# Kernel optimization log

Hardware: AMD Instinct MI355X
Metric: run time of the kernel (lower is better)

## Reference

```python
import jax, jax.numpy as jnp
import numpy as np

H = 8          # num_heads
EPS = 1e-5     # nn.LayerNorm default eps


def _attn(x, kv, wq, bq, wk, bk, wv, bv, wo, bo):
    # x: [B, Nq, D] queries; kv: [B, Nk, D] keys/values. softmax over keys (dim=-1).
    B, Nq, D = x.shape
    Nk = kv.shape[1]
    d = D // H
    q = (x @ wq + bq).reshape(B, Nq, H, d).transpose(0, 2, 1, 3)   # [B,h,Nq,d]
    k = (kv @ wk + bk).reshape(B, Nk, H, d).transpose(0, 2, 1, 3)  # [B,h,Nk,d]
    v = (kv @ wv + bv).reshape(B, Nk, H, d).transpose(0, 2, 1, 3)  # [B,h,Nk,d]
    scores = jnp.einsum('bhqd,bhkd->bhqk', q, k) * (d ** -0.5)
    a = jax.nn.softmax(scores, axis=-1)                            # softmax_dim='keys'
    ctx = jnp.einsum('bhqk,bhkd->bhqd', a, v)
    ctx = ctx.transpose(0, 2, 1, 3).reshape(B, Nq, D)
    return ctx @ wo + bo


def _ln(x, g, b):
    mu = jnp.mean(x, axis=-1, keepdims=True)
    var = jnp.var(x, axis=-1, keepdims=True)  # biased, matches torch LayerNorm
    return (x - mu) * jax.lax.rsqrt(var + EPS) * g + b


def setup_inputs() -> dict:
    key = jax.random.key(0)
    B, Nq, Nk, D = 2, 2048, 4096, 512
    Hid = 4 * D
    ks = jax.random.split(key, 32)
    s = 0.02
    r = lambda i, shp: jax.random.normal(ks[i], shp, dtype=jnp.float32) * s
    inp = {
        'x': jax.random.normal(ks[0], (B, Nq, D), dtype=jnp.float32),
        'cross': jax.random.normal(ks[1], (B, Nk, D), dtype=jnp.float32),
        # cross-attention projections (stored as [in, out])
        'ca_wq': r(2, (D, D)), 'ca_bq': jnp.zeros((D,), jnp.float32),
        'ca_wk': r(3, (D, D)), 'ca_bk': jnp.zeros((D,), jnp.float32),
        'ca_wv': r(4, (D, D)), 'ca_bv': jnp.zeros((D,), jnp.float32),
        'ca_wo': r(5, (D, D)), 'ca_bo': jnp.zeros((D,), jnp.float32),
        # self-attention projections
        'sa_wq': r(6, (D, D)), 'sa_bq': jnp.zeros((D,), jnp.float32),
        'sa_wk': r(7, (D, D)), 'sa_bk': jnp.zeros((D,), jnp.float32),
        'sa_wv': r(8, (D, D)), 'sa_bv': jnp.zeros((D,), jnp.float32),
        'sa_wo': r(9, (D, D)), 'sa_bo': jnp.zeros((D,), jnp.float32),
        # layer norms
        'ln1_g': jnp.ones((D,), jnp.float32), 'ln1_b': jnp.zeros((D,), jnp.float32),
        'ln2_g': jnp.ones((D,), jnp.float32), 'ln2_b': jnp.zeros((D,), jnp.float32),
        # MLP
        'mlp_w1': r(10, (D, Hid)), 'mlp_b1': jnp.zeros((Hid,), jnp.float32),
        'mlp_w2': r(11, (Hid, D)), 'mlp_b2': jnp.zeros((D,), jnp.float32),
    }
    return inp


def reference(x, cross,
              ca_wq, ca_bq, ca_wk, ca_bk, ca_wv, ca_bv, ca_wo, ca_bo,
              sa_wq, sa_bq, sa_wk, sa_bk, sa_wv, sa_bv, sa_wo, sa_bo,
              ln1_g, ln1_b, ln2_g, ln2_b,
              mlp_w1, mlp_b1, mlp_w2, mlp_b2):
    # a) cross-attention
    xc = _attn(x, cross, ca_wq, ca_bq, ca_wk, ca_bk, ca_wv, ca_bv, ca_wo, ca_bo)
    # b,c) LN then self-attention (Q=K=V=ln1(xc))
    xn = _ln(xc, ln1_g, ln1_b)
    xs = _attn(xn, xn, sa_wq, sa_bq, sa_wk, sa_bk, sa_wv, sa_bv, sa_wo, sa_bo)
    # d) residual
    y = xc + xs
    # e,f) LN + GELU MLP (torch GELU default = exact erf)
    h1 = jax.nn.gelu(_ln(y, ln2_g, ln2_b) @ mlp_w1 + mlp_b1, approximate=False)
    z = h1 @ mlp_w2 + mlp_b2
    # g) residual
    return y + z
```

## Files before the change

kernel.cpp:

```cpp
#include <hip/hip_runtime.h>
#include <math.h>

typedef _Float16 f16;
typedef __attribute__((ext_vector_type(8))) _Float16 f16x8;
typedef __attribute__((ext_vector_type(4))) _Float16 f16x4;
typedef __attribute__((ext_vector_type(4))) float f32x4;
typedef __attribute__((ext_vector_type(2))) __fp16 h16x2;

#define QSCALE 0.1803368801111204f

__device__ __forceinline__ void gl_lds16(const f16* g, f16* l) {
    __builtin_amdgcn_global_load_lds((const __attribute__((address_space(1))) void*)g,
                                     (__attribute__((address_space(3))) void*)l, 16, 0, 0);
}

struct PrepArgs {
    const float* ws[10]; f16* wd[10];
    const float* x; f16* xh;
    const float* cross; f16* ch;
};
__global__ __launch_bounds__(256)
void prep_all(PrepArgs p) {
    __shared__ float t[32][33];
    int bid = blockIdx.x, tid = threadIdx.x;
    if (bid < 4096) {
        const float* W; f16* Wt; int K, N, nx, ky;
        if (bid < 2048) {
            int wi = bid >> 8, tl = bid & 255;
            W = p.ws[wi]; Wt = p.wd[wi]; K = 512; N = 512; nx = tl & 15; ky = tl >> 4;
        } else if (bid < 3072) {
            int tl = bid - 2048;
            W = p.ws[8]; Wt = p.wd[8]; K = 512; N = 2048; nx = tl & 63; ky = tl >> 6;
        } else {
            int tl = bid - 3072;
            W = p.ws[9]; Wt = p.wd[9]; K = 2048; N = 512; nx = tl & 15; ky = tl >> 4;
        }
        int tx = tid & 31, ty = tid >> 5;
        int n0 = nx * 32, k0 = ky * 32;
#pragma unroll
        for (int i = 0; i < 4; i++)
            t[ty + i * 8][tx] = W[(size_t)(k0 + ty + i * 8) * N + n0 + tx];
        __syncthreads();
#pragma unroll
        for (int i = 0; i < 4; i++)
            Wt[(size_t)(n0 + ty + i * 8) * K + k0 + tx] = (f16)t[tx][ty + i * 8];
    } else {
        const float* X; f16* Y; size_t cb;
        if (bid < 6144) { X = p.x; Y = p.xh; cb = bid - 4096; }
        else            { X = p.cross; Y = p.ch; cb = bid - 6144; }
        size_t i = (cb * 256 + tid) * 4;
        f32x4 v = *(const f32x4*)(X + i);
        f16x4 o;
        o[0] = (f16)v[0]; o[1] = (f16)v[1]; o[2] = (f16)v[2]; o[3] = (f16)v[3];
        *(f16x4*)(Y + i) = o;
    }
}

__global__ __launch_bounds__(256)
void transpose_v(const f16* __restrict__ Vh, f16* __restrict__ Vt, int Nk) {
    __shared__ f16 t[64][72];
    int bh = blockIdx.y, k0 = blockIdx.x * 64;
    int tid = threadIdx.x;
    int kr = tid >> 2, dc = (tid & 3) * 16;
    const f16* src = Vh + ((size_t)bh * Nk + k0 + kr) * 64 + dc;
    f16x8 a = *(const f16x8*)src;
    f16x8 b = *(const f16x8*)(src + 8);
    *(f16x8*)&t[kr][dc] = a;
    *(f16x8*)&t[kr][dc + 8] = b;
    __syncthreads();
    int dr = tid >> 2, kc = (tid & 3) * 16;
    f16x8 o0, o1;
#pragma unroll
    for (int j = 0; j < 8; j++) { o0[j] = t[kc + j][dr]; o1[j] = t[kc + 8 + j][dr]; }
    f16* dst = Vt + ((size_t)bh * 64 + dr) * Nk + k0 + kc;
    *(f16x8*)dst = o0;
    *(f16x8*)(dst + 8) = o1;
}

__global__ __launch_bounds__(128)
void layernorm_f16(const float* __restrict__ X, const float* __restrict__ g,
                   const float* __restrict__ bta, f16* __restrict__ Y)
{
    __shared__ float red[4];
    int row = blockIdx.x;
    int tid = threadIdx.x;
    const float* x = X + (size_t)row * 512;
    f32x4 v = *(const f32x4*)(x + tid * 4);
    float s  = v[0] + v[1] + v[2] + v[3];
    float ss = v[0] * v[0] + v[1] * v[1] + v[2] * v[2] + v[3] * v[3];
#pragma unroll
    for (int m = 1; m < 64; m <<= 1) {
        s  += __shfl_xor(s, m, 64);
        ss += __shfl_xor(ss, m, 64);
    }
    int wave = tid >> 6, lane = tid & 63;
    if (lane == 0) { red[wave * 2] = s; red[wave * 2 + 1] = ss; }
    __syncthreads();
    s = red[0] + red[2]; ss = red[1] + red[3];
    float mu  = s * (1.0f / 512);
    float var = ss * (1.0f / 512) - mu * mu;
    float inv = rsqrtf(var + 1e-5f);
    f32x4 gv = *(const f32x4*)(g + tid * 4);
    f32x4 bv = *(const f32x4*)(bta + tid * 4);
    f16x4 o;
#pragma unroll
    for (int i = 0; i < 4; i++) o[i] = (f16)((v[i] - mu) * inv * gv[i] + bv[i]);
    *(f16x4*)(Y + (size_t)row * 512 + tid * 4) = o;
}

__global__ __launch_bounds__(256)
void gemm_f16(const f16* __restrict__ A, const f16* __restrict__ Wt,
              const float* __restrict__ b0, const float* __restrict__ b1,
              const float* __restrict__ b2, const float* __restrict__ res,
              float* __restrict__ Cf32, f16* __restrict__ C16,
              f16* __restrict__ hm0, f16* __restrict__ hm1, f16* __restrict__ hm2,
              int N, int K, int NBshift, int fused, int act, float s0)
{
    __shared__ __align__(16) f16 As[128 * 64];
    __shared__ __align__(16) f16 Bs[128 * 64];
    int tid = threadIdx.x, lane = tid & 63, wave = tid >> 6;
    int quad = lane >> 4, ln16 = lane & 15;
    int wm = wave >> 1, wn = wave & 1;
    int bm0 = blockIdx.y * 128, bn0 = blockIdx.x * 128;

    f32x4 acc[4][4];
#pragma unroll
    for (int i = 0; i < 4; i++)
#pragma unroll
        for (int j = 0; j < 4; j++) acc[i][j] = (f32x4){0.f, 0.f, 0.f, 0.f};

    const f16* ag[4]; const f16* bg[4]; f16* al[4]; f16* bl[4];
#pragma unroll
    for (int j = 0; j < 4; j++) {
        int L = tid + j * 256;
        int row = L >> 3, cc = (L & 7) ^ (row & 7);
        ag[j] = A  + (size_t)(bm0 + row) * K + cc * 8;
        bg[j] = Wt + (size_t)(bn0 + row) * K + cc * 8;
        al[j] = As + (size_t)L * 8;
        bl[j] = Bs + (size_t)L * 8;
    }
    int sw0 = (quad ^ (ln16 & 7)) * 8, sw1 = ((4 + quad) ^ (ln16 & 7)) * 8;

    for (int kt = 0; kt < K; kt += 64) {
        __syncthreads();
#pragma unroll
        for (int j = 0; j < 4; j++) gl_lds16(ag[j], al[j]);
#pragma unroll
        for (int j = 0; j < 4; j++) gl_lds16(bg[j], bl[j]);
        __syncthreads();
#pragma unroll
        for (int h = 0; h < 2; h++) {
            int sw = h ? sw1 : sw0;
            f16x8 af[4], bf[4];
#pragma unroll
            for (int mt = 0; mt < 4; mt++)
                af[mt] = *(const f16x8*)&As[(wm * 64 + mt * 16 + ln16) * 64 + sw];
#pragma unroll
            for (int nt = 0; nt < 4; nt++)
                bf[nt] = *(const f16x8*)&Bs[(wn * 64 + nt * 16 + ln16) * 64 + sw];
#pragma unroll
            for (int mt = 0; mt < 4; mt++)
#pragma unroll
                for (int nt = 0; nt < 4; nt++)
                    acc[mt][nt] = __builtin_amdgcn_mfma_f32_16x16x32_f16(af[mt], bf[nt], acc[mt][nt], 0, 0, 0);
        }
#pragma unroll
        for (int j = 0; j < 4; j++) { ag[j] += 64; bg[j] += 64; }
    }

    int NB = 1 << NBshift;
#pragma unroll
    for (int mt = 0; mt < 4; mt++) {
#pragma unroll
        for (int nt = 0; nt < 4; nt++) {
            int row = bm0 + wm * 64 + mt * 16 + quad * 4;
            int col = bn0 + wn * 64 + nt * 16 + ln16;
            float bv;
            if (fused) {
                int seg = col >> 9;
                const float* bp = seg == 0 ? b0 : (seg == 1 ? b1 : b2);
                bv = bp[col & 511];
            } else bv = b0[col];
#pragma unroll
            for (int i = 0; i < 4; i++) {
                int r = row + i;
                float v = acc[mt][nt][i] + bv;
                size_t idx = (size_t)r * N + col;
                if (res) v += res[idx];
                if (act) v = 0.5f * v * (1.0f + erff(v * 0.70710678118654752f));
                if (Cf32) Cf32[idx] = v;
                if (C16) C16[idx] = (f16)v;
                if (hm0) {
                    int seg = col >> 9;
                    f16* hp = seg == 0 ? hm0 : (seg == 1 ? hm1 : hm2);
                    float vv = seg == 0 ? v * s0 : v;
                    int hh = (col >> 6) & 7, d = col & 63;
                    int bt = r >> NBshift, rr = r & (NB - 1);
                    hp[(((size_t)bt * 8 + hh) * NB + rr) * 64 + d] = (f16)vv;
                }
            }
        }
    }
}

__global__ __launch_bounds__(256)
void gemm64(const f16* __restrict__ A, const f16* __restrict__ Wt,
            const float* __restrict__ bias, const float* __restrict__ res,
            float* __restrict__ Cf32, f16* __restrict__ hm0,
            int N, int K, int NBshift, float s0)
{
    __shared__ __align__(16) f16 As[2][64 * 64];
    __shared__ __align__(16) f16 Bs[2][64 * 64];
    int tid = threadIdx.x, lane = tid & 63, wave = tid >> 6;
    int quad = lane >> 4, ln16 = lane & 15;
    int wm = wave >> 1, wn = wave & 1;
    int bm0 = blockIdx.y * 64, bn0 = blockIdx.x * 64;

    f32x4 acc[2][2];
#pragma unroll
    for (int i = 0; i < 2; i++)
#pragma unroll
        for (int j = 0; j < 2; j++) acc[i][j] = (f32x4){0.f, 0.f, 0.f, 0.f};

    const f16* ag[2]; const f16* bg[2]; int Loff[2];
#pragma unroll
    for (int j = 0; j < 2; j++) {
        int L = tid + j * 256;
        int row = L >> 3, cc = (L & 7) ^ (row & 7);
        ag[j] = A  + (size_t)(bm0 + row) * K + cc * 8;
        bg[j] = Wt + (size_t)(bn0 + row) * K + cc * 8;
        Loff[j] = L * 8;
    }
    int sw0 = (quad ^ (ln16 & 7)) * 8, sw1 = ((4 + quad) ^ (ln16 & 7)) * 8;

#pragma unroll
    for (int j = 0; j < 2; j++) { gl_lds16(ag[j], &As[0][Loff[j]]); gl_lds16(bg[j], &Bs[0][Loff[j]]); }
#pragma unroll
    for (int j = 0; j < 2; j++) { ag[j] += 64; bg[j] += 64; }

    int cur = 0;
    for (int kt = 0; kt < K; kt += 64) {
        __syncthreads();
        if (kt + 64 < K) {
            int nxt = cur ^ 1;
#pragma unroll
            for (int j = 0; j < 2; j++) { gl_lds16(ag[j], &As[nxt][Loff[j]]); gl_lds16(bg[j], &Bs[nxt][Loff[j]]); }
#pragma unroll
            for (int j = 0; j < 2; j++) { ag[j] += 64; bg[j] += 64; }
        }
        const f16* Ac = As[cur]; const f16* Bc = Bs[cur];
#pragma unroll
        for (int h = 0; h < 2; h++) {
            int sw = h ? sw1 : sw0;
            f16x8 af[2], bf[2];
#pragma unroll
            for (int mt = 0; mt < 2; mt++)
                af[mt] = *(const f16x8*)&Ac[(wm * 32 + mt * 16 + ln16) * 64 + sw];
#pragma unroll
            for (int nt = 0; nt < 2; nt++)
                bf[nt] = *(const f16x8*)&Bc[(wn * 32 + nt * 16 + ln16) * 64 + sw];
#pragma unroll
            for (int mt = 0; mt < 2; mt++)
#pragma unroll
                for (int nt = 0; nt < 2; nt++)
                    acc[mt][nt] = __builtin_amdgcn_mfma_f32_16x16x32_f16(af[mt], bf[nt], acc[mt][nt], 0, 0, 0);
        }
        cur ^= 1;
    }

    int NB = 1 << NBshift;
#pragma unroll
    for (int mt = 0; mt < 2; mt++) {
#pragma unroll
        for (int nt = 0; nt < 2; nt++) {
            int row = bm0 + wm * 32 + mt * 16 + quad * 4;
            int col = bn0 + wn * 32 + nt * 16 + ln16;
            float bv = bias[col];
#pragma unroll
            for (int i = 0; i < 4; i++) {
                int r = row + i;
                float v = acc[mt][nt][i] + bv;
                size_t idx = (size_t)r * N + col;
                if (res) v += res[idx];
                if (Cf32) Cf32[idx] = v;
                if (hm0) {
                    int hh = (col >> 6) & 7, d = col & 63;
                    int bt = r >> NBshift, rr = r & (NB - 1);
                    hm0[(((size_t)bt * 8 + hh) * NB + rr) * 64 + d] = (f16)(v * s0);
                }
            }
        }
    }
}

__global__ __launch_bounds__(512, 4)
void attention_split(const f16* __restrict__ Qh, const f16* __restrict__ Kh,
                     const f16* __restrict__ Vt, f16* __restrict__ Op,
                     float* __restrict__ Lsum, int Nk)
{
    __shared__ __align__(16) f16 Kt[64 * 64];
    __shared__ __align__(16) f16 Vs[64 * 64];
    __shared__ __align__(16) f16 Ps[8 * 32 * 64];
    int z = blockIdx.z, b = z >> 2, sp = z & 3;
    int h = blockIdx.y, bh = b * 8 + h;
    int Nkh = Nk >> 2;
    int tid = threadIdx.x, lane = tid & 63, wave = tid >> 6;
    int quad = lane >> 4, ln16 = lane & 15, l7 = ln16 & 7;
    int qrow0 = blockIdx.x * 256 + wave * 32;

    f16x8 qf[2][2];
#pragma unroll
    for (int qh = 0; qh < 2; qh++)
#pragma unroll
        for (int dh = 0; dh < 2; dh++)
            qf[qh][dh] = *(const f16x8*)(Qh + ((size_t)bh * 2048 + qrow0 + qh * 16 + ln16) * 64
                                         + dh * 32 + quad * 8);
    f16x8 ones;
#pragma unroll
    for (int j = 0; j < 8; j++) ones[j] = (f16)1.0f;

    f32x4 oacc[2][4], aol[2];
#pragma unroll
    for (int qh = 0; qh < 2; qh++) {
        aol[qh] = (f32x4){0.f, 0.f, 0.f, 0.f};
#pragma unroll
        for (int dt = 0; dt < 4; dt++) oacc[qh][dt] = (f32x4){0.f, 0.f, 0.f, 0.f};
    }

    const f16* kb = Kh + ((size_t)bh * Nk + sp * Nkh) * 64;
    const f16* vb = Vt + (size_t)bh * 64 * Nk + sp * Nkh;

    const f16* kg; const f16* vg; f16* kl; f16* vl;
    {
        int L = tid;
        int row = L >> 3, cc = (L & 7) ^ (row & 7);
        kg = kb + (size_t)row * 64 + cc * 8;
        vg = vb + (size_t)row * Nk + cc * 8;
        kl = Kt + (size_t)L * 8;
        vl = Vs + (size_t)L * 8;
    }

    int koff[4][2], voff[4][2], poff_r[2][2];
#pragma unroll
    for (int nt = 0; nt < 4; nt++)
#pragma unroll
        for (int dh = 0; dh < 2; dh++)
            koff[nt][dh] = (nt * 16 + ln16) * 64 + ((dh * 4 + quad) ^ l7) * 8;
#pragma unroll
    for (int dt = 0; dt < 4; dt++)
#pragma unroll
        for (int c = 0; c < 2; c++)
            voff[dt][c] = (dt * 16 + ln16) * 64 + ((c * 4 + quad) ^ l7) * 8;
    int pbase = wave * 2048;
#pragma unroll
    for (int qh = 0; qh < 2; qh++)
#pragma unroll
        for (int c = 0; c < 2; c++)
            poff_r[qh][c] = pbase + (qh * 16 + ln16) * 64 + ((c * 4 + quad) ^ l7) * 8;
    int pw_half = (quad & 1) * 4;
    int pw_rowc = quad >> 1;

    for (int kt = 0; kt < Nkh; kt += 64) {
        __syncthreads();
        gl_lds16(kg, kl);
        gl_lds16(vg, vl);
        __syncthreads();
        kg += 64 * 64; vg += 64;

        {
            f16x8 kf[4][2];
#pragma unroll
            for (int nt = 0; nt < 4; nt++)
#pragma unroll
                for (int dh = 0; dh < 2; dh++)
                    kf[nt][dh] = *(const f16x8*)&Kt[koff[nt][dh]];
#pragma unroll
            for (int qh = 0; qh < 2; qh++) {
                int prow = pbase + (qh * 16 + ln16) * 64;
#pragma unroll
                for (int nt = 0; nt < 4; nt++) {
                    f32x4 zz = (f32x4){0.f, 0.f, 0.f, 0.f};
                    zz = __builtin_amdgcn_mfma_f32_16x16x32_f16(kf[nt][0], qf[qh][0], zz, 0, 0, 0);
                    zz = __builtin_amdgcn_mfma_f32_16x16x32_f16(kf[nt][1], qf[qh][1], zz, 0, 0, 0);
                    float e0 = exp2f(zz[0]), e1 = exp2f(zz[1]);
                    float e2 = exp2f(zz[2]), e3 = exp2f(zz[3]);
                    h16x2 pa = __builtin_amdgcn_cvt_pkrtz(e0, e1);
                    h16x2 pb = __builtin_amdgcn_cvt_pkrtz(e2, e3);
                    union { h16x2 h[2]; f16x4 v; } u;
                    u.h[0] = pa; u.h[1] = pb;
                    *(f16x4*)&Ps[prow + ((nt * 2 + pw_rowc) ^ l7) * 8 + pw_half] = u.v;
                }
            }
        }
        {
            f16x8 vf[4][2];
#pragma unroll
            for (int dt = 0; dt < 4; dt++)
#pragma unroll
                for (int c = 0; c < 2; c++)
                    vf[dt][c] = *(const f16x8*)&Vs[voff[dt][c]];
#pragma unroll
            for (int qh = 0; qh < 2; qh++) {
                f16x8 pf0 = *(const f16x8*)&Ps[poff_r[qh][0]];
                f16x8 pf1 = *(const f16x8*)&Ps[poff_r[qh][1]];
                aol[qh] = __builtin_amdgcn_mfma_f32_16x16x32_f16(ones, pf0, aol[qh], 0, 0, 0);
                aol[qh] = __builtin_amdgcn_mfma_f32_16x16x32_f16(ones, pf1, aol[qh], 0, 0, 0);
#pragma unroll
                for (int dt = 0; dt < 4; dt++) {
                    oacc[qh][dt] = __builtin_amdgcn_mfma_f32_16x16x32_f16(vf[dt][0], pf0, oacc[qh][dt], 0, 0, 0);
                    oacc[qh][dt] = __builtin_amdgcn_mfma_f32_16x16x32_f16(vf[dt][1], pf1, oacc[qh][dt], 0, 0, 0);
                }
            }
        }
    }

#pragma unroll
    for (int qh = 0; qh < 2; qh++) {
        size_t rowb = ((size_t)(sp * 16 + bh) * 2048 + qrow0 + qh * 16 + ln16) * 64;
#pragma unroll
        for (int dt = 0; dt < 4; dt++) {
            f16x4 o4;
#pragma unroll
            for (int i = 0; i < 4; i++) o4[i] = (f16)oacc[qh][dt][i];
            *(f16x4*)&Op[rowb + dt * 16 + quad * 4] = o4;
        }
        if (quad == 0)
            Lsum[(size_t)(sp * 16 + bh) * 2048 + qrow0 + qh * 16 + ln16] = aol[qh][0];
    }
}

__global__ __launch_bounds__(256)
void attn_combine(const f16* __restrict__ Op, const float* __restrict__ Lsum,
                  f16* __restrict__ O)
{
    int t = blockIdx.x * 256 + threadIdx.x;
    int d = t & 63;
    int q = (t >> 6) & 2047;
    int bh = t >> 17;
    int b = bh >> 3, h = bh & 7;
    float l = 0.f, val = 0.f;
#pragma unroll
    for (int s = 0; s < 4; s++) {
        l   += Lsum[(size_t)(s * 16 + bh) * 2048 + q];
        val += (float)Op[((size_t)(s * 16 + bh) * 2048 + q) * 64 + d];
    }
    O[((size_t)b * 2048 + q) * 512 + h * 64 + d] = (f16)(val / l);
}

extern "C" void kernel_launch(void* const* d_in, const int* in_sizes, int n_in,
                              void* d_out, int out_size, void* d_ws, size_t ws_size,
                              hipStream_t stream)
{
    (void)in_sizes; (void)n_in; (void)out_size; (void)ws_size;
    const float* x      = (const float*)d_in[0];
    const float* cross  = (const float*)d_in[1];
    const float* ca_wq  = (const float*)d_in[2];
    const float* ca_bq  = (const float*)d_in[3];
    const float* ca_wk  = (const float*)d_in[4];
    const float* ca_bk  = (const float*)d_in[5];
    const float* ca_wv  = (const float*)d_in[6];
    const float* ca_bv  = (const float*)d_in[7];
    const float* ca_wo  = (const float*)d_in[8];
    const float* ca_bo  = (const float*)d_in[9];
    const float* sa_wq  = (const float*)d_in[10];
    const float* sa_bq  = (const float*)d_in[11];
    const float* sa_wk  = (const float*)d_in[12];
    const float* sa_bk  = (const float*)d_in[13];
    const float* sa_wv  = (const float*)d_in[14];
    const float* sa_bv  = (const float*)d_in[15];
    const float* sa_wo  = (const float*)d_in[16];
    const float* sa_bo  = (const float*)d_in[17];
    const float* ln1_g  = (const float*)d_in[18];
    const float* ln1_b  = (const float*)d_in[19];
    const float* ln2_g  = (const float*)d_in[20];
    const float* ln2_b  = (const float*)d_in[21];
    const float* mlp_w1 = (const float*)d_in[22];
    const float* mlp_b1 = (const float*)d_in[23];
    const float* mlp_w2 = (const float*)d_in[24];
    const float* mlp_b2 = (const float*)d_in[25];
    float* out = (float*)d_out;

    float* XC = (float*)d_ws;
    float* Yb = XC + 2097152;
    f16* fb   = (f16*)(Yb + 2097152);
    f16* xh     = fb;
    f16* crossh = xh + 2097152;
    f16* xnh    = crossh + 4194304;
    f16* xn2h   = xnh + 2097152;
    f16* Qh     = xn2h + 2097152;
    f16* Kh     = Qh + 2097152;
    f16* Vh     = Kh + 4194304;
    f16* Vtb    = Vh + 4194304;
    f16* ctxh   = Vtb + 4194304;
    f16* h1h    = ctxh + 2097152;
    f16* t_caq  = h1h + 8388608;
    f16* t_cak  = t_caq + 262144;
    f16* t_cav  = t_cak + 262144;
    f16* t_cao  = t_cav + 262144;
    f16* t_saq  = t_cao + 262144;
    f16* t_sak  = t_saq + 262144;
    f16* t_sav  = t_sak + 262144;
    f16* t_sao  = t_sav + 262144;
    f16* t_w1   = t_sao + 262144;
    f16* t_w2   = t_w1 + 1048576;
    float* Lsum = (float*)(t_w2 + 1048576);

    PrepArgs pa;
    pa.ws[0] = ca_wq; pa.wd[0] = t_caq;
    pa.ws[1] = ca_wk; pa.wd[1] = t_cak;
    pa.ws[2] = ca_wv; pa.wd[2] = t_cav;
    pa.ws[3] = ca_wo; pa.wd[3] = t_cao;
    pa.ws[4] = sa_wq; pa.wd[4] = t_saq;
    pa.ws[5] = sa_wk; pa.wd[5] = t_sak;
    pa.ws[6] = sa_wv; pa.wd[6] = t_sav;
    pa.ws[7] = sa_wo; pa.wd[7] = t_sao;
    pa.ws[8] = mlp_w1; pa.wd[8] = t_w1;
    pa.ws[9] = mlp_w2; pa.wd[9] = t_w2;
    pa.x = x; pa.xh = xh; pa.cross = cross; pa.ch = crossh;
    prep_all<<<10240, 256, 0, stream>>>(pa);

    gemm64<<<dim3(8, 64), 256, 0, stream>>>(xh, t_caq, ca_bq, nullptr, nullptr, Qh,
                                            512, 512, 11, QSCALE);
    gemm_f16<<<dim3(8, 64), 256, 0, stream>>>(crossh, t_cak, ca_bk, ca_bv, nullptr, nullptr,
        nullptr, nullptr, Kh, Vh, nullptr, 1024, 512, 12, 1, 0, 1.0f);
    transpose_v<<<dim3(64, 16), 256, 0, stream>>>(Vh, Vtb, 4096);
    attention_split<<<dim3(8, 8, 8), 512, 0, stream>>>(Qh, Kh, Vtb, h1h, Lsum, 4096);
    attn_combine<<<8192, 256, 0, stream>>>(h1h, Lsum, ctxh);
    gemm64<<<dim3(8, 64), 256, 0, stream>>>(ctxh, t_cao, ca_bo, nullptr, XC, nullptr,
                                            512, 512, 11, 1.0f);
    layernorm_f16<<<4096, 128, 0, stream>>>(XC, ln1_g, ln1_b, xnh);
    gemm_f16<<<dim3(12, 32), 256, 0, stream>>>(xnh, t_saq, sa_bq, sa_bk, sa_bv, nullptr,
        nullptr, nullptr, Qh, Kh, Vh, 1536, 512, 11, 1, 0, QSCALE);
    transpose_v<<<dim3(32, 16), 256, 0, stream>>>(Vh, Vtb, 2048);
    attention_split<<<dim3(8, 8, 8), 512, 0, stream>>>(Qh, Kh, Vtb, h1h, Lsum, 2048);
    attn_combine<<<8192, 256, 0, stream>>>(h1h, Lsum, ctxh);
    gemm64<<<dim3(8, 64), 256, 0, stream>>>(ctxh, t_sao, sa_bo, XC, Yb, nullptr,
                                            512, 512, 11, 1.0f);
    layernorm_f16<<<4096, 128, 0, stream>>>(Yb, ln2_g, ln2_b, xn2h);
    gemm_f16<<<dim3(16, 32), 256, 0, stream>>>(xn2h, t_w1, mlp_b1, nullptr, nullptr, nullptr,
        nullptr, h1h, nullptr, nullptr, nullptr, 2048, 512, 11, 0, 1, 1.0f);
    gemm64<<<dim3(8, 64), 256, 0, stream>>>(h1h, t_w2, mlp_b2, Yb, out, nullptr,
                                            512, 2048, 11, 1.0f);
}
```

Before: 367.4 us.

## Double-buffer LDS tiles in GEMM and attention; keep softmax P in registers

Both the GEMM and the split-key attention kernels now use two LDS buffers. The next K-tile's global-to-LDS load is issued before computing on the current tile, and one barrier per iteration replaces two. The attention kernel also drops the per-wave Ps LDS staging of exponentiated scores. It feeds the packed f16 P fragments straight from registers into 16x16x16 MFMAs, which removes an LDS write and read per tile. The cost is doubled LDS footprint, more MFMA instructions of smaller K, and higher register pressure under launch_bounds(512,4).

```diff
diff --git a/kernel.cpp b/kernel.cpp
--- a/kernel.cpp
+++ b/kernel.cpp
@@ -116,8 +116,8 @@
               f16* __restrict__ hm0, f16* __restrict__ hm1, f16* __restrict__ hm2,
               int N, int K, int NBshift, int fused, int act, float s0)
 {
-    __shared__ __align__(16) f16 As[128 * 64];
-    __shared__ __align__(16) f16 Bs[128 * 64];
+    __shared__ __align__(16) f16 As[2][128 * 64];
+    __shared__ __align__(16) f16 Bs[2][128 * 64];
     int tid = threadIdx.x, lane = tid & 63, wave = tid >> 6;
     int quad = lane >> 4, ln16 = lane & 15;
     int wm = wave >> 1, wn = wave & 1;
@@ -129,43 +129,50 @@
 #pragma unroll
         for (int j = 0; j < 4; j++) acc[i][j] = (f32x4){0.f, 0.f, 0.f, 0.f};
 
-    const f16* ag[4]; const f16* bg[4]; f16* al[4]; f16* bl[4];
+    const f16* ag[4]; const f16* bg[4]; int Loff[4];
 #pragma unroll
     for (int j = 0; j < 4; j++) {
         int L = tid + j * 256;
         int row = L >> 3, cc = (L & 7) ^ (row & 7);
         ag[j] = A  + (size_t)(bm0 + row) * K + cc * 8;
         bg[j] = Wt + (size_t)(bn0 + row) * K + cc * 8;
-        al[j] = As + (size_t)L * 8;
-        bl[j] = Bs + (size_t)L * 8;
+        Loff[j] = L * 8;
     }
     int sw0 = (quad ^ (ln16 & 7)) * 8, sw1 = ((4 + quad) ^ (ln16 & 7)) * 8;
 
+#pragma unroll
+    for (int j = 0; j < 4; j++) { gl_lds16(ag[j], &As[0][Loff[j]]); gl_lds16(bg[j], &Bs[0][Loff[j]]); }
+#pragma unroll
+    for (int j = 0; j < 4; j++) { ag[j] += 64; bg[j] += 64; }
+
+    int cur = 0;
     for (int kt = 0; kt < K; kt += 64) {
         __syncthreads();
-#pragma unroll
-        for (int j = 0; j < 4; j++) gl_lds16(ag[j], al[j]);
-#pragma unroll
-        for (int j = 0; j < 4; j++) gl_lds16(bg[j], bl[j]);
-        __syncthreads();
+        if (kt + 64 < K) {
+            int nxt = cur ^ 1;
+#pragma unroll
+            for (int j = 0; j < 4; j++) { gl_lds16(ag[j], &As[nxt][Loff[j]]); gl_lds16(bg[j], &Bs[nxt][Loff[j]]); }
+#pragma unroll
+            for (int j = 0; j < 4; j++) { ag[j] += 64; bg[j] += 64; }
+        }
+        const f16* Ac = As[cur]; const f16* Bc = Bs[cur];
 #pragma unroll
         for (int h = 0; h < 2; h++) {
             int sw = h ? sw1 : sw0;
             f16x8 af[4], bf[4];
 #pragma unroll
             for (int mt = 0; mt < 4; mt++)
-                af[mt] = *(const f16x8*)&As[(wm * 64 + mt * 16 + ln16) * 64 + sw];
+                af[mt] = *(const f16x8*)&Ac[(wm * 64 + mt * 16 + ln16) * 64 + sw];
 #pragma unroll
             for (int nt = 0; nt < 4; nt++)
-                bf[nt] = *(const f16x8*)&Bs[(wn * 64 + nt * 16 + ln16) * 64 + sw];
+                bf[nt] = *(const f16x8*)&Bc[(wn * 64 + nt * 16 + ln16) * 64 + sw];
 #pragma unroll
             for (int mt = 0; mt < 4; mt++)
 #pragma unroll
                 for (int nt = 0; nt < 4; nt++)
                     acc[mt][nt] = __builtin_amdgcn_mfma_f32_16x16x32_f16(af[mt], bf[nt], acc[mt][nt], 0, 0, 0);
         }
-#pragma unroll
-        for (int j = 0; j < 4; j++) { ag[j] += 64; bg[j] += 64; }
+        cur ^= 1;
     }
 
     int NB = 1 << NBshift;
@@ -298,9 +305,8 @@
                      const f16* __restrict__ Vt, f16* __restrict__ Op,
                      float* __restrict__ Lsum, int Nk)
 {
-    __shared__ __align__(16) f16 Kt[64 * 64];
-    __shared__ __align__(16) f16 Vs[64 * 64];
-    __shared__ __align__(16) f16 Ps[8 * 32 * 64];
+    __shared__ __align__(16) f16 Kt[2][64 * 64];
+    __shared__ __align__(16) f16 Vs[2][64 * 64];
     int z = blockIdx.z, b = z >> 2, sp = z & 3;
     int h = blockIdx.y, bh = b * 8 + h;
     int Nkh = Nk >> 2;
@@ -315,9 +321,9 @@
         for (int dh = 0; dh < 2; dh++)
             qf[qh][dh] = *(const f16x8*)(Qh + ((size_t)bh * 2048 + qrow0 + qh * 16 + ln16) * 64
                                          + dh * 32 + quad * 8);
-    f16x8 ones;
-#pragma unroll
-    for (int j = 0; j < 8; j++) ones[j] = (f16)1.0f;
+    f16x4 ones4;
+#pragma unroll
+    for (int j = 0; j < 4; j++) ones4[j] = (f16)1.0f;
 
     f32x4 oacc[2][4], aol[2];
 #pragma unroll
@@ -330,17 +336,16 @@
     const f16* kb = Kh + ((size_t)bh * Nk + sp * Nkh) * 64;
     const f16* vb = Vt + (size_t)bh * 64 * Nk + sp * Nkh;
 
-    const f16* kg; const f16* vg; f16* kl; f16* vl;
+    const f16* kg; const f16* vg; int Lo;
     {
         int L = tid;
         int row = L >> 3, cc = (L & 7) ^ (row & 7);
         kg = kb + (size_t)row * 64 + cc * 8;
         vg = vb + (size_t)row * Nk + cc * 8;
-        kl = Kt + (size_t)L * 8;
-        vl = Vs + (size_t)L * 8;
-    }
-
-    int koff[4][2], voff[4][2], poff_r[2][2];
+        Lo = L * 8;
+    }
+
+    int koff[4][2], voff16[4][4];
 #pragma unroll
     for (int nt = 0; nt < 4; nt++)
 #pragma unroll
@@ -349,69 +354,66 @@
 #pragma unroll
     for (int dt = 0; dt < 4; dt++)
 #pragma unroll
-        for (int c = 0; c < 2; c++)
-            voff[dt][c] = (dt * 16 + ln16) * 64 + ((c * 4 + quad) ^ l7) * 8;
-    int pbase = wave * 2048;
-#pragma unroll
-    for (int qh = 0; qh < 2; qh++)
-#pragma unroll
-        for (int c = 0; c < 2; c++)
-            poff_r[qh][c] = pbase + (qh * 16 + ln16) * 64 + ((c * 4 + quad) ^ l7) * 8;
-    int pw_half = (quad & 1) * 4;
-    int pw_rowc = quad >> 1;
-
+        for (int nt = 0; nt < 4; nt++)
+            voff16[dt][nt] = (dt * 16 + ln16) * 64 + (((nt * 2 + (quad >> 1)) ^ l7) * 8) + (quad & 1) * 4;
+
+    gl_lds16(kg, &Kt[0][Lo]);
+    gl_lds16(vg, &Vs[0][Lo]);
+    kg += 64 * 64; vg += 64;
+
+    int cur = 0;
     for (int kt = 0; kt < Nkh; kt += 64) {
         __syncthreads();
-        gl_lds16(kg, kl);
-        gl_lds16(vg, vl);
-        __syncthreads();
-        kg += 64 * 64; vg += 64;
-
+        if (kt + 64 < Nkh) {
+            int nxt = cur ^ 1;
+            gl_lds16(kg, &Kt[nxt][Lo]);
+            gl_lds16(vg, &Vs[nxt][Lo]);
+            kg += 64 * 64; vg += 64;
+        }
+        const f16* Ktc = Kt[cur]; const f16* Vsc = Vs[cur];
+
+        f16x4 pk[2][4];
         {
             f16x8 kf[4][2];
 #pragma unroll
             for (int nt = 0; nt < 4; nt++)
 #pragma unroll
                 for (int dh = 0; dh < 2; dh++)
-                    kf[nt][dh] = *(const f16x8*)&Kt[koff[nt][dh]];
-#pragma unroll
-            for (int qh = 0; qh < 2; qh++) {
-                int prow = pbase + (qh * 16 + ln16) * 64;
+                    kf[nt][dh] = *(const f16x8*)&Ktc[koff[nt][dh]];
+#pragma unroll
+            for (int qh = 0; qh < 2; qh++)
 #pragma unroll
                 for (int nt = 0; nt < 4; nt++) {
                     f32x4 zz = (f32x4){0.f, 0.f, 0.f, 0.f};
                     zz = __builtin_amdgcn_mfma_f32_16x16x32_f16(kf[nt][0], qf[qh][0], zz, 0, 0, 0);
                     zz = __builtin_amdgcn_mfma_f32_16x16x32_f16(kf[nt][1], qf[qh][1], zz, 0, 0, 0);
-                    float e0 = exp2f(zz[0]), e1 = exp2f(zz[1]);
-                    float e2 = exp2f(zz[2]), e3 = exp2f(zz[3]);
-                    h16x2 pa = __builtin_amdgcn_cvt_pkrtz(e0, e1);
-                    h16x2 pb = __builtin_amdgcn_cvt_pkrtz(e2, e3);
+                    h16x2 pa = __builtin_amdgcn_cvt_pkrtz(exp2f(zz[0]), exp2f(zz[1]));
+                    h16x2 pb = __builtin_amdgcn_cvt_pkrtz(exp2f(zz[2]), exp2f(zz[3]));
                     union { h16x2 h[2]; f16x4 v; } u;
                     u.h[0] = pa; u.h[1] = pb;
-                    *(f16x4*)&Ps[prow + ((nt * 2 + pw_rowc) ^ l7) * 8 + pw_half] = u.v;
+                    pk[qh][nt] = u.v;
                 }
+        }
+        {
+            f16x4 vf[4][4];
+#pragma unroll
+            for (int dt = 0; dt < 4; dt++)
+#pragma unroll
+                for (int nt = 0; nt < 4; nt++)
+                    vf[dt][nt] = *(const f16x4*)&Vsc[voff16[dt][nt]];
+#pragma unroll
+            for (int qh = 0; qh < 2; qh++) {
+#pragma unroll
+                for (int nt = 0; nt < 4; nt++)
+                    aol[qh] = __builtin_amdgcn_mfma_f32_16x16x16f16(ones4, pk[qh][nt], aol[qh], 0, 0, 0);
+#pragma unroll
+                for (int dt = 0; dt < 4; dt++)
+#pragma unroll
+                    for (int nt = 0; nt < 4; nt++)
+                        oacc[qh][dt] = __builtin_amdgcn_mfma_f32_16x16x16f16(vf[dt][nt], pk[qh][nt], oacc[qh][dt], 0, 0, 0);
             }
         }
-        {
-            f16x8 vf[4][2];
-#pragma unroll
-            for (int dt = 0; dt < 4; dt++)
-#pragma unroll
-                for (int c = 0; c < 2; c++)
-                    vf[dt][c] = *(const f16x8*)&Vs[voff[dt][c]];
-#pragma unroll
-            for (int qh = 0; qh < 2; qh++) {
-                f16x8 pf0 = *(const f16x8*)&Ps[poff_r[qh][0]];
-                f16x8 pf1 = *(const f16x8*)&Ps[poff_r[qh][1]];
-                aol[qh] = __builtin_amdgcn_mfma_f32_16x16x32_f16(ones, pf0, aol[qh], 0, 0, 0);
-                aol[qh] = __builtin_amdgcn_mfma_f32_16x16x32_f16(ones, pf1, aol[qh], 0, 0, 0);
-#pragma unroll
-                for (int dt = 0; dt < 4; dt++) {
-                    oacc[qh][dt] = __builtin_amdgcn_mfma_f32_16x16x32_f16(vf[dt][0], pf0, oacc[qh][dt], 0, 0, 0);
-                    oacc[qh][dt] = __builtin_amdgcn_mfma_f32_16x16x32_f16(vf[dt][1], pf1, oacc[qh][dt], 0, 0, 0);
-                }
-            }
-        }
+        cur ^= 1;
     }
 
 #pragma unroll
```

New measurement: 365.3 us. No clear change (-0.6%).
